# Optimization experiments

Hardware: AMD Instinct MI355X
Metric: run time of the kernel (lower is better)

## Reference

```python
import jax, jax.numpy as jnp
import numpy as np

N_RAYS = 32768
N_OBJ = 16
N_SAMPLES = 32   # n_pts_object
N_BASE = 64      # pre-existing coarse samples per ray
MISS = 1e10      # sentinel for non-intersecting slots (sorts to the end)


def _make_transforms(key):
    """Random rigid+scale world-to-object transforms, pytorch3d row-vector convention:
    p' = p @ M[:3,:3] + M[3,:3]."""
    k1, k2, k3 = jax.random.split(key, 3)
    A = jax.random.normal(k1, (N_OBJ, 3, 3))
    Q, _ = jnp.linalg.qr(A)                                   # orthonormal 3x3
    t = jax.random.normal(k2, (N_OBJ, 3)) * 5.0               # translations
    s = jax.random.uniform(k3, (N_OBJ, 3), minval=0.5, maxval=2.0)
    eye = jnp.tile(jnp.eye(4, dtype=jnp.float32), (N_OBJ, 1, 1))
    rots = eye.at[:, :3, :3].set(Q.astype(jnp.float32))
    trafos = rots.at[:, 3, :3].set(t)
    scales = eye.at[:, 0, 0].set(s[:, 0]).at[:, 1, 1].set(s[:, 1]).at[:, 2, 2].set(s[:, 2])
    return trafos, rots, scales


def setup_inputs() -> dict:
    key = jax.random.key(0)
    k0, k1, k2, k3 = jax.random.split(key, 4)
    origins = jax.random.normal(k0, (N_RAYS, 3), dtype=jnp.float32) * 2.0
    directions = jax.random.normal(k1, (N_RAYS, 3), dtype=jnp.float32)
    lengths = jnp.sort(jax.random.uniform(k2, (N_RAYS, N_BASE), dtype=jnp.float32,
                                          minval=0.1, maxval=20.0), axis=-1)
    trafos, rots, scales = _make_transforms(k3)
    return {"origins": origins, "directions": directions, "lengths": lengths,
            "trafos_w2o": trafos, "rots_w2o": rots, "scales_w2o": scales}


def reference(origins, directions, lengths, trafos_w2o, rots_w2o, scales_w2o):
    N = origins.shape[0]
    M = trafos_w2o.shape[0]
    S = N_SAMPLES

    d_w = directions / jnp.linalg.norm(directions, axis=-1, keepdims=True)

    # compose transforms (row-vector convention: compose(m1, m2) -> m1 @ m2)
    pt_mat = trafos_w2o @ scales_w2o     # points world->object, [M,4,4]
    dir_mat = rots_w2o @ scales_w2o      # directions world->object

    # rays in each object frame: [M,N,3]
    origins_o = jnp.einsum('ni,mij->mnj', origins, pt_mat[:, :3, :3]) + pt_mat[:, None, 3, :3]
    dirs_o = jnp.einsum('ni,mij->mnj', d_w, dir_mat[:, :3, :3])
    dirs_o = dirs_o / jnp.linalg.norm(dirs_o, axis=-1, keepdims=True)

    # slab ray-AABB intersection against unit box [-1,1]^3
    inv = 1.0 / dirs_o
    t0 = (-1.0 - origins_o) * inv
    t1 = (1.0 - origins_o) * inv
    tmin = jnp.max(jnp.minimum(t0, t1), axis=-1)   # [M,N]
    tmax = jnp.min(jnp.maximum(t0, t1), axis=-1)
    hit = (tmax > tmin) & (tmax > 0.0)
    t_in = jnp.maximum(tmin, 0.0)

    # BoxRaysampler: linspace between entry and exit
    lin = jnp.linspace(0.0, 1.0, S, dtype=origins.dtype)
    z_o = t_in[..., None] + (tmax - t_in)[..., None] * lin          # [M,N,S]

    # object-space sample points / dirs
    pts_o = origins_o[:, :, None] + dirs_o[:, :, None] * z_o[..., None]   # [M,N,S,3]
    dirs_o_s = jnp.broadcast_to(dirs_o[:, :, None], pts_o.shape)

    # back to world -> z along world ray
    o2w = jnp.linalg.inv(pt_mat)
    pts_w = jnp.einsum('mnsi,mij->mnsj', pts_o, o2w[:, :3, :3]) + o2w[:, None, None, 3, :3]
    z_w = jnp.einsum('mnsj,nj->mns', pts_w - origins[None, :, None], d_w)
    z_w = jnp.where(hit[..., None], z_w, MISS)                      # mask misses

    # scatter into per-ray lengths (static worst-case size), then sort per ray
    z_flat = jnp.transpose(z_w, (1, 0, 2)).reshape(N, M * S)        # [N, M*S]
    lengths_new = jnp.concatenate([lengths, z_flat], axis=-1)       # [N, B+M*S]

    node_ids = jnp.broadcast_to(jnp.arange(M, dtype=jnp.int32)[:, None, None], (M, N, S))
    node_ids = jnp.where(hit[..., None], node_ids, -1)
    node_flat = jnp.concatenate(
        [jnp.full((N, lengths.shape[-1]), -1, dtype=jnp.int32),
         jnp.transpose(node_ids, (1, 0, 2)).reshape(N, M * S)], axis=-1)
    mask_flat = jnp.concatenate(
        [jnp.zeros((N, lengths.shape[-1]), dtype=bool),
         jnp.transpose(jnp.broadcast_to(hit[..., None], (M, N, S)), (1, 0, 2)).reshape(N, M * S)],
        axis=-1)

    order = jnp.argsort(lengths_new, axis=-1)
    sorted_lengths = jnp.take_along_axis(lengths_new, order, axis=-1)
    sorted_nodes = jnp.take_along_axis(node_flat, order, axis=-1)
    sorted_mask = jnp.take_along_axis(mask_flat, order, axis=-1)

    # flattened object-space samples (zeroed for misses; static shape)
    pts_flat = (pts_o * hit[..., None, None]).reshape(-1, 3)
    dirs_flat = (dirs_o_s * hit[..., None, None]).reshape(-1, 3)

    return sorted_lengths, sorted_nodes, sorted_mask, pts_flat, dirs_flat
```

## Files before the change

kernel.cpp:

```cpp
#include <hip/hip_runtime.h>

#define NR    32768
#define NOBJ  16
#define NS    32
#define NB    64
#define WIDTH 576
#define MISSV 1e10f

__device__ __forceinline__ float fmulr(float a, float b){ return __fmul_rn(a,b); }
__device__ __forceinline__ float faddr(float a, float b){ return __fadd_rn(a,b); }
__device__ __forceinline__ float fsubr(float a, float b){ return __fsub_rn(a,b); }
__device__ __forceinline__ float fdvr (float a, float b){ return __fdiv_rn(a,b); }

struct RayObj {
  float oo[3];
  float dd[3];
  float t_in, dt;
  float dn;
  bool  hit;
};

__device__ __forceinline__ void ray_obj_setup(
    const float* __restrict__ origins, const float* __restrict__ dirs,
    const float* __restrict__ trafos,  const float* __restrict__ scales,
    int m, int n, RayObj& R)
{
  const float o0 = origins[3*n+0], o1 = origins[3*n+1], o2 = origins[3*n+2];
  const float r0 = dirs[3*n+0],    r1 = dirs[3*n+1],    r2 = dirs[3*n+2];
  const float nn = __fsqrt_rn(faddr(faddr(fmulr(r0,r0), fmulr(r1,r1)), fmulr(r2,r2)));
  const float w0 = fdvr(r0,nn), w1 = fdvr(r1,nn), w2 = fdvr(r2,nn);

  const float* T = trafos + 16*m;
  const float* S = scales + 16*m;
  const float s0 = S[0], s1 = S[5], s2 = S[10];
  const float pm00 = fmulr(T[0],  s0), pm01 = fmulr(T[1],  s1), pm02 = fmulr(T[2],  s2);
  const float pm10 = fmulr(T[4],  s0), pm11 = fmulr(T[5],  s1), pm12 = fmulr(T[6],  s2);
  const float pm20 = fmulr(T[8],  s0), pm21 = fmulr(T[9],  s1), pm22 = fmulr(T[10], s2);
  const float tm0  = fmulr(T[12], s0), tm1  = fmulr(T[13], s1), tm2  = fmulr(T[14], s2);

  const float oo0 = faddr(faddr(faddr(fmulr(o0,pm00), fmulr(o1,pm10)), fmulr(o2,pm20)), tm0);
  const float oo1 = faddr(faddr(faddr(fmulr(o0,pm01), fmulr(o1,pm11)), fmulr(o2,pm21)), tm1);
  const float oo2 = faddr(faddr(faddr(fmulr(o0,pm02), fmulr(o1,pm12)), fmulr(o2,pm22)), tm2);
  const float du0 = faddr(faddr(fmulr(w0,pm00), fmulr(w1,pm10)), fmulr(w2,pm20));
  const float du1 = faddr(faddr(fmulr(w0,pm01), fmulr(w1,pm11)), fmulr(w2,pm21));
  const float du2 = faddr(faddr(fmulr(w0,pm02), fmulr(w1,pm12)), fmulr(w2,pm22));
  const float dn  = __fsqrt_rn(faddr(faddr(fmulr(du0,du0), fmulr(du1,du1)), fmulr(du2,du2)));
  const float dd0 = fdvr(du0,dn), dd1 = fdvr(du1,dn), dd2 = fdvr(du2,dn);

  const float i0 = fdvr(1.0f, dd0), i1 = fdvr(1.0f, dd1), i2 = fdvr(1.0f, dd2);
  const float a0 = fmulr(fsubr(-1.0f, oo0), i0), b0 = fmulr(fsubr(1.0f, oo0), i0);
  const float a1 = fmulr(fsubr(-1.0f, oo1), i1), b1 = fmulr(fsubr(1.0f, oo1), i1);
  const float a2 = fmulr(fsubr(-1.0f, oo2), i2), b2 = fmulr(fsubr(1.0f, oo2), i2);
  const float tmn = fmaxf(fmaxf(fminf(a0,b0), fminf(a1,b1)), fminf(a2,b2));
  const float tmx = fminf(fminf(fmaxf(a0,b0), fmaxf(a1,b1)), fmaxf(a2,b2));

  R.hit  = (tmx > tmn) && (tmx > 0.0f);
  R.t_in = fmaxf(tmn, 0.0f);
  R.dt   = fsubr(tmx, R.t_in);
  R.dn   = dn;
  R.oo[0]=oo0; R.oo[1]=oo1; R.oo[2]=oo2;
  R.dd[0]=dd0; R.dd[1]=dd1; R.dd[2]=dd2;
}

__global__ __launch_bounds__(256) void k_ptsdirs(
    const float* __restrict__ origins, const float* __restrict__ dirs,
    const float* __restrict__ trafos,  const float* __restrict__ scales,
    float* __restrict__ outP, float* __restrict__ outD)
{
  __shared__ __align__(16) float ld[64][8];
  const int tid = threadIdx.x;
  const int m   = blockIdx.x >> 9;
  const int n0  = (blockIdx.x & 511) << 6;
  if (tid < 64) {
    RayObj R;
    ray_obj_setup(origins, dirs, trafos, scales, m, n0 + tid, R);
    const bool h = R.hit;
    ld[tid][0] = h ? R.oo[0] : 0.0f;
    ld[tid][1] = h ? R.oo[1] : 0.0f;
    ld[tid][2] = h ? R.oo[2] : 0.0f;
    ld[tid][3] = h ? R.dd[0] : 0.0f;
    ld[tid][4] = h ? R.dd[1] : 0.0f;
    ld[tid][5] = h ? R.t_in  : 0.0f;
    ld[tid][6] = h ? R.dt    : 0.0f;
    ld[tid][7] = h ? R.dd[2] : 0.0f;
  }
  __syncthreads();
  const size_t base = (size_t)(m * NR + n0) * 96;
  float4* P4 = (float4*)(outP + base);
  float4* D4 = (float4*)(outD + base);
  #pragma unroll
  for (int it = 0; it < 6; ++it) {
    const int f   = tid + (it << 8);
    const int rr  = f / 24;
    const int off = (f - rr * 24) * 4;
    const float oox = ld[rr][0], ooy = ld[rr][1], ooz = ld[rr][2];
    const float ddx = ld[rr][3], ddy = ld[rr][4], ddz = ld[rr][7];
    const float ti  = ld[rr][5], dtt = ld[rr][6];
    float4 p, d;
    float* pp = (float*)&p; float* dv = (float*)&d;
    #pragma unroll
    for (int i = 0; i < 4; ++i) {
      const int idx = off + i;
      const int s   = idx / 3;
      const int c   = idx - s * 3;
      const float z  = ti + dtt * ((float)s * (1.0f/31.0f));
      const float oc = (c == 0) ? oox : ((c == 1) ? ooy : ooz);
      const float dc = (c == 0) ? ddx : ((c == 1) ? ddy : ddz);
      pp[i] = oc + dc * z;
      dv[i] = dc;
    }
    P4[f] = p;
    D4[f] = d;
  }
}

__device__ __forceinline__ int count_run(const float* __restrict__ K,
                                         const float* __restrict__ A,
                                         const float* __restrict__ B,
                                         const float* __restrict__ IB,
                                         int m2, float key, bool tie)
{
  const float A2 = A[m2], B2 = B[m2];
  const float* V = K + NB + m2 * NS;
  if (B2 <= 0.0f) {
    return (A2 < key || (A2 == key && tie)) ? NS : 0;
  }
  float g = floorf(fmulr(fsubr(key, A2), IB[m2]));
  g = fminf(33.0f, fmaxf(-1.0f, g));
  int c = (int)g + 1;
  c = c < 0 ? 0 : (c > NS ? NS : c);
  while (c > 0)  { const float v = V[c-1]; if (v < key || (v == key && tie)) break; --c; }
  while (c < NS) { const float v = V[c];   if (v < key || (v == key && tie)) ++c; else break; }
  return c;
}

__global__ __launch_bounds__(256) void k_sort(
    const float* __restrict__ origins, const float* __restrict__ dirs,
    const float* __restrict__ lengths,
    const float* __restrict__ trafos,  const float* __restrict__ scales,
    float* __restrict__ outL, float* __restrict__ outN, float* __restrict__ outM)
{
  __shared__ __align__(16) float sKeys[4][WIDTH];
  __shared__ __align__(16) float sA[4][NOBJ], sB[4][NOBJ], sIB[4][NOBJ];
  __shared__ __align__(16) float sL[4][WIDTH], sN[4][WIDTH];

  const int tid  = threadIdx.x;
  const int wv   = tid >> 6;
  const int lane = tid & 63;
  const int n    = blockIdx.x * 4 + wv;

  if (lane < NOBJ) {
    RayObj R;
    ray_obj_setup(origins, dirs, trafos, scales, lane, n, R);
    float myA = MISSV, myB = -1.0f, myIB = 0.0f;
    if (R.hit) {
      const double invdn = 1.0 / (double)R.dn;
      myA = (float)((double)R.t_in * invdn);
      myB = (float)(((double)R.dt * invdn) * (1.0 / 31.0));
      if (!(myB > 0.0f)) myB = 0.0f;
      myIB = (myB > 0.0f) ? (1.0f / myB) : 0.0f;
    }
    sA[wv][lane]  = myA;
    sB[wv][lane]  = R.hit ? myB : -1.0f;
    sIB[wv][lane] = myIB;
  }
  __syncthreads();

  unsigned hm = 0;
  #pragma unroll
  for (int mm = 0; mm < NOBJ; ++mm) hm |= (sB[wv][mm] >= 0.0f ? 1u : 0u) << mm;
  const int H = __popc(hm);

  float kr[9];
  kr[0] = lengths[n * NB + lane];
  sKeys[wv][lane] = kr[0];
  #pragma unroll
  for (int k = 1; k < 9; ++k) {
    const int m0 = 2*(k-1) + (lane >> 5);
    const int s  = lane & 31;
    const float A_ = sA[wv][m0], B_ = sB[wv][m0];
    const float key = (B_ < 0.0f) ? MISSV : faddr(A_, fmulr(B_, (float)s));
    kr[k] = key;
    sKeys[wv][64*k + lane] = key;
  }
  __syncthreads();

  const float* K = sKeys[wv];
  #pragma unroll
  for (int k = 0; k < 9; ++k) {
    const float key = kr[k];
    int rank; float nodef; float outkey = key;
    if (k == 0) {
      rank = lane;
      unsigned mm = hm;
      while (mm) { const int m2 = __ffs(mm) - 1; mm &= mm - 1;
        rank += count_run(K, sA[wv], sB[wv], sIB[wv], m2, key, false); }
      nodef = -1.0f;
    } else {
      const int m = 2*(k-1) + (lane >> 5);
      const int s = lane & 31;
      if (!((hm >> m) & 1u)) {
        const int MB = __popc((~hm) & ((1u << m) - 1u) & 0xFFFFu);
        rank  = NB + NS*H + NS*MB + s;
        nodef = -1.0f; outkey = MISSV;
      } else {
        rank = s;
        int c = 0;
        #pragma unroll
        for (int st = 64; st >= 1; st >>= 1) {
          const int t2 = c + st;
          if (t2 <= NB && K[t2-1] <= key) c = t2;
        }
        rank += c;
        unsigned mm = hm & ~(1u << m);
        while (mm) { const int m2 = __ffs(mm) - 1; mm &= mm - 1;
          rank += count_run(K, sA[wv], sB[wv], sIB[wv], m2, key, m2 < m); }
        nodef = (float)m;
      }
    }
    sL[wv][rank] = outkey;
    sN[wv][rank] = nodef;
  }
  __syncthreads();

  float4* pL = (float4*)(outL + (size_t)n * WIDTH);
  float4* pN = (float4*)(outN + (size_t)n * WIDTH);
  float4* pM = (float4*)(outM + (size_t)n * WIDTH);
  const float4* qL = (const float4*)sL[wv];
  const float4* qN = (const float4*)sN[wv];
  for (int i = lane; i < WIDTH/4; i += 64) pL[i] = qL[i];
  for (int i = lane; i < WIDTH/4; i += 64) {
    const float4 nv = qN[i];
    float4 mv;
    mv.x = nv.x >= 0.0f ? 1.0f : 0.0f;
    mv.y = nv.y >= 0.0f ? 1.0f : 0.0f;
    mv.z = nv.z >= 0.0f ? 1.0f : 0.0f;
    mv.w = nv.w >= 0.0f ? 1.0f : 0.0f;
    pN[i] = nv;
    pM[i] = mv;
  }
}

extern "C" void kernel_launch(void* const* d_in, const int* in_sizes, int n_in,
                              void* d_out, int out_size, void* d_ws, size_t ws_size,
                              hipStream_t stream)
{
  (void)in_sizes; (void)n_in; (void)out_size; (void)d_ws; (void)ws_size;
  const float* origins = (const float*)d_in[0];
  const float* dirs    = (const float*)d_in[1];
  const float* lengths = (const float*)d_in[2];
  const float* trafos  = (const float*)d_in[3];
  const float* scales  = (const float*)d_in[5];

  float* out  = (float*)d_out;
  float* outL = out;
  float* outN = out + (size_t)NR * WIDTH;
  float* outM = out + (size_t)2 * NR * WIDTH;
  float* outP = out + (size_t)3 * NR * WIDTH;
  float* outD = outP + (size_t)NOBJ * NR * NS * 3;

  hipLaunchKernelGGL(k_ptsdirs, dim3(NOBJ * 512), dim3(256), 0, stream,
                     origins, dirs, trafos, scales, outP, outD);
  hipLaunchKernelGGL(k_sort, dim3(NR / 4), dim3(256), 0, stream,
                     origins, dirs, lengths, trafos, scales, outL, outN, outM);
}
```

Measured before the change: 627.9 us.

## Fuse point generation and sort kernels into one interleaved launch

Merges the points/directions kernel and the per-ray sort kernel into a single kernel whose blocks alternate roles by block index parity, sharing LDS through a union. This is meant to overlap the bandwidth-heavy point writes with the latency-heavy sort work and remove the gap between two launches. In exchange, point blocks inherit the sort kernel's register and shared-memory footprint, which may reduce their occupancy.

```diff
diff --git a/kernel.cpp b/kernel.cpp
--- a/kernel.cpp
+++ b/kernel.cpp
@@ -62,58 +62,6 @@
   R.dd[0]=dd0; R.dd[1]=dd1; R.dd[2]=dd2;
 }
 
-__global__ __launch_bounds__(256) void k_ptsdirs(
-    const float* __restrict__ origins, const float* __restrict__ dirs,
-    const float* __restrict__ trafos,  const float* __restrict__ scales,
-    float* __restrict__ outP, float* __restrict__ outD)
-{
-  __shared__ __align__(16) float ld[64][8];
-  const int tid = threadIdx.x;
-  const int m   = blockIdx.x >> 9;
-  const int n0  = (blockIdx.x & 511) << 6;
-  if (tid < 64) {
-    RayObj R;
-    ray_obj_setup(origins, dirs, trafos, scales, m, n0 + tid, R);
-    const bool h = R.hit;
-    ld[tid][0] = h ? R.oo[0] : 0.0f;
-    ld[tid][1] = h ? R.oo[1] : 0.0f;
-    ld[tid][2] = h ? R.oo[2] : 0.0f;
-    ld[tid][3] = h ? R.dd[0] : 0.0f;
-    ld[tid][4] = h ? R.dd[1] : 0.0f;
-    ld[tid][5] = h ? R.t_in  : 0.0f;
-    ld[tid][6] = h ? R.dt    : 0.0f;
-    ld[tid][7] = h ? R.dd[2] : 0.0f;
-  }
-  __syncthreads();
-  const size_t base = (size_t)(m * NR + n0) * 96;
-  float4* P4 = (float4*)(outP + base);
-  float4* D4 = (float4*)(outD + base);
-  #pragma unroll
-  for (int it = 0; it < 6; ++it) {
-    const int f   = tid + (it << 8);
-    const int rr  = f / 24;
-    const int off = (f - rr * 24) * 4;
-    const float oox = ld[rr][0], ooy = ld[rr][1], ooz = ld[rr][2];
-    const float ddx = ld[rr][3], ddy = ld[rr][4], ddz = ld[rr][7];
-    const float ti  = ld[rr][5], dtt = ld[rr][6];
-    float4 p, d;
-    float* pp = (float*)&p; float* dv = (float*)&d;
-    #pragma unroll
-    for (int i = 0; i < 4; ++i) {
-      const int idx = off + i;
-      const int s   = idx / 3;
-      const int c   = idx - s * 3;
-      const float z  = ti + dtt * ((float)s * (1.0f/31.0f));
-      const float oc = (c == 0) ? oox : ((c == 1) ? ooy : ooz);
-      const float dc = (c == 0) ? ddx : ((c == 1) ? ddy : ddz);
-      pp[i] = oc + dc * z;
-      dv[i] = dc;
-    }
-    P4[f] = p;
-    D4[f] = d;
-  }
-}
-
 __device__ __forceinline__ int count_run(const float* __restrict__ K,
                                          const float* __restrict__ A,
                                          const float* __restrict__ B,
@@ -134,20 +82,76 @@
   return c;
 }
 
-__global__ __launch_bounds__(256) void k_sort(
+struct PtsS  { float ld[64][8]; };
+struct SortS {
+  float sKeys[4][WIDTH];
+  float sA[4][NOBJ], sB[4][NOBJ], sIB[4][NOBJ];
+  float sL[4][WIDTH], sN[4][WIDTH];
+};
+union __align__(16) Smem { PtsS p; SortS s; };
+
+__global__ __launch_bounds__(256) void k_fused(
     const float* __restrict__ origins, const float* __restrict__ dirs,
     const float* __restrict__ lengths,
     const float* __restrict__ trafos,  const float* __restrict__ scales,
-    float* __restrict__ outL, float* __restrict__ outN, float* __restrict__ outM)
-{
-  __shared__ __align__(16) float sKeys[4][WIDTH];
-  __shared__ __align__(16) float sA[4][NOBJ], sB[4][NOBJ], sIB[4][NOBJ];
-  __shared__ __align__(16) float sL[4][WIDTH], sN[4][WIDTH];
-
+    float* __restrict__ outL, float* __restrict__ outN, float* __restrict__ outM,
+    float* __restrict__ outP, float* __restrict__ outD)
+{
+  __shared__ Smem U;
   const int tid  = threadIdx.x;
+  const int role = blockIdx.x & 1;
+  const int bid  = blockIdx.x >> 1;
+
+  if (role == 0) {
+    const int m   = bid >> 9;
+    const int n0  = (bid & 511) << 6;
+    if (tid < 64) {
+      RayObj R;
+      ray_obj_setup(origins, dirs, trafos, scales, m, n0 + tid, R);
+      const bool h = R.hit;
+      U.p.ld[tid][0] = h ? R.oo[0] : 0.0f;
+      U.p.ld[tid][1] = h ? R.oo[1] : 0.0f;
+      U.p.ld[tid][2] = h ? R.oo[2] : 0.0f;
+      U.p.ld[tid][3] = h ? R.dd[0] : 0.0f;
+      U.p.ld[tid][4] = h ? R.dd[1] : 0.0f;
+      U.p.ld[tid][5] = h ? R.t_in  : 0.0f;
+      U.p.ld[tid][6] = h ? R.dt    : 0.0f;
+      U.p.ld[tid][7] = h ? R.dd[2] : 0.0f;
+    }
+    __syncthreads();
+    const size_t base = (size_t)(m * NR + n0) * 96;
+    float4* P4 = (float4*)(outP + base);
+    float4* D4 = (float4*)(outD + base);
+    #pragma unroll
+    for (int it = 0; it < 6; ++it) {
+      const int f   = tid + (it << 8);
+      const int rr  = f / 24;
+      const int off = (f - rr * 24) * 4;
+      const float oox = U.p.ld[rr][0], ooy = U.p.ld[rr][1], ooz = U.p.ld[rr][2];
+      const float ddx = U.p.ld[rr][3], ddy = U.p.ld[rr][4], ddz = U.p.ld[rr][7];
+      const float ti  = U.p.ld[rr][5], dtt = U.p.ld[rr][6];
+      float4 p, d;
+      float* pp = (float*)&p; float* dv = (float*)&d;
+      #pragma unroll
+      for (int i = 0; i < 4; ++i) {
+        const int idx = off + i;
+        const int s   = idx / 3;
+        const int c   = idx - s * 3;
+        const float z  = ti + dtt * ((float)s * (1.0f/31.0f));
+        const float oc = (c == 0) ? oox : ((c == 1) ? ooy : ooz);
+        const float dc = (c == 0) ? ddx : ((c == 1) ? ddy : ddz);
+        pp[i] = oc + dc * z;
+        dv[i] = dc;
+      }
+      P4[f] = p;
+      D4[f] = d;
+    }
+    return;
+  }
+
   const int wv   = tid >> 6;
   const int lane = tid & 63;
-  const int n    = blockIdx.x * 4 + wv;
+  const int n    = bid * 4 + wv;
 
   if (lane < NOBJ) {
     RayObj R;
@@ -160,32 +164,32 @@
       if (!(myB > 0.0f)) myB = 0.0f;
       myIB = (myB > 0.0f) ? (1.0f / myB) : 0.0f;
     }
-    sA[wv][lane]  = myA;
-    sB[wv][lane]  = R.hit ? myB : -1.0f;
-    sIB[wv][lane] = myIB;
+    U.s.sA[wv][lane]  = myA;
+    U.s.sB[wv][lane]  = R.hit ? myB : -1.0f;
+    U.s.sIB[wv][lane] = myIB;
   }
   __syncthreads();
 
   unsigned hm = 0;
   #pragma unroll
-  for (int mm = 0; mm < NOBJ; ++mm) hm |= (sB[wv][mm] >= 0.0f ? 1u : 0u) << mm;
+  for (int mm = 0; mm < NOBJ; ++mm) hm |= (U.s.sB[wv][mm] >= 0.0f ? 1u : 0u) << mm;
   const int H = __popc(hm);
 
   float kr[9];
   kr[0] = lengths[n * NB + lane];
-  sKeys[wv][lane] = kr[0];
+  U.s.sKeys[wv][lane] = kr[0];
   #pragma unroll
   for (int k = 1; k < 9; ++k) {
     const int m0 = 2*(k-1) + (lane >> 5);
     const int s  = lane & 31;
-    const float A_ = sA[wv][m0], B_ = sB[wv][m0];
+    const float A_ = U.s.sA[wv][m0], B_ = U.s.sB[wv][m0];
     const float key = (B_ < 0.0f) ? MISSV : faddr(A_, fmulr(B_, (float)s));
     kr[k] = key;
-    sKeys[wv][64*k + lane] = key;
+    U.s.sKeys[wv][64*k + lane] = key;
   }
   __syncthreads();
 
-  const float* K = sKeys[wv];
+  const float* K = U.s.sKeys[wv];
   #pragma unroll
   for (int k = 0; k < 9; ++k) {
     const float key = kr[k];
@@ -194,7 +198,7 @@
       rank = lane;
       unsigned mm = hm;
       while (mm) { const int m2 = __ffs(mm) - 1; mm &= mm - 1;
-        rank += count_run(K, sA[wv], sB[wv], sIB[wv], m2, key, false); }
+        rank += count_run(K, U.s.sA[wv], U.s.sB[wv], U.s.sIB[wv], m2, key, false); }
       nodef = -1.0f;
     } else {
       const int m = 2*(k-1) + (lane >> 5);
@@ -214,20 +218,20 @@
         rank += c;
         unsigned mm = hm & ~(1u << m);
         while (mm) { const int m2 = __ffs(mm) - 1; mm &= mm - 1;
-          rank += count_run(K, sA[wv], sB[wv], sIB[wv], m2, key, m2 < m); }
+          rank += count_run(K, U.s.sA[wv], U.s.sB[wv], U.s.sIB[wv], m2, key, m2 < m); }
         nodef = (float)m;
       }
     }
-    sL[wv][rank] = outkey;
-    sN[wv][rank] = nodef;
+    U.s.sL[wv][rank] = outkey;
+    U.s.sN[wv][rank] = nodef;
   }
   __syncthreads();
 
   float4* pL = (float4*)(outL + (size_t)n * WIDTH);
   float4* pN = (float4*)(outN + (size_t)n * WIDTH);
   float4* pM = (float4*)(outM + (size_t)n * WIDTH);
-  const float4* qL = (const float4*)sL[wv];
-  const float4* qN = (const float4*)sN[wv];
+  const float4* qL = (const float4*)U.s.sL[wv];
+  const float4* qN = (const float4*)U.s.sN[wv];
   for (int i = lane; i < WIDTH/4; i += 64) pL[i] = qL[i];
   for (int i = lane; i < WIDTH/4; i += 64) {
     const float4 nv = qN[i];
@@ -259,8 +263,7 @@
   float* outP = out + (size_t)3 * NR * WIDTH;
   float* outD = outP + (size_t)NOBJ * NR * NS * 3;
 
-  hipLaunchKernelGGL(k_ptsdirs, dim3(NOBJ * 512), dim3(256), 0, stream,
-                     origins, dirs, trafos, scales, outP, outD);
-  hipLaunchKernelGGL(k_sort, dim3(NR / 4), dim3(256), 0, stream,
-                     origins, dirs, lengths, trafos, scales, outL, outN, outM);
-}
+  hipLaunchKernelGGL(k_fused, dim3(16384), dim3(256), 0, stream,
+                     origins, dirs, lengths, trafos, scales,
+                     outL, outN, outM, outP, outD);
+}
```

Measured after the change: 623.3 us. Within noise of the previous version (-0.7%).
